# Performance work log

Measured on AMD Instinct MI355X. Metric: run time of the kernel, lower is better.

The kernel has to match this reference:

```python
import jax, jax.numpy as jnp
import numpy as np

B, T, D, H, F, E, K = 4, 1024, 1024, 16, 2048, 8, 2
LN_EPS = 1e-6  # flax LayerNorm default


def setup_inputs() -> dict:
    key = jax.random.key(0)
    ks = jax.random.split(key, 8)
    s = 0.02
    return {
        "x": jax.random.normal(ks[0], (B, T, D), jnp.float32),
        "ln1_scale": jnp.ones((D,), jnp.float32),
        "ln1_bias": jnp.zeros((D,), jnp.float32),
        "qkv_w": jax.random.normal(ks[1], (D, 3 * D), jnp.float32) * s,
        "qkv_b": jnp.zeros((3 * D,), jnp.float32),
        "out_w": jax.random.normal(ks[2], (D, D), jnp.float32) * s,
        "out_b": jnp.zeros((D,), jnp.float32),
        "ln2_scale": jnp.ones((D,), jnp.float32),
        "ln2_bias": jnp.zeros((D,), jnp.float32),
        "router_w": jax.random.normal(ks[3], (D, E), jnp.float32) * s,
        "w1": jax.random.normal(ks[4], (E, D, F), jnp.float32) * s,
        "b1": jnp.zeros((E, F), jnp.float32),
        "w2": jax.random.normal(ks[5], (E, F, D), jnp.float32) * s,
        "b2": jnp.zeros((E, D), jnp.float32),
    }


def _layernorm(x, scale, bias):
    mu = jnp.mean(x, axis=-1, keepdims=True)
    var = jnp.mean(jnp.square(x - mu), axis=-1, keepdims=True)
    return (x - mu) * jax.lax.rsqrt(var + LN_EPS) * scale + bias


def _attention(x, qkv_w, qkv_b, out_w, out_b):
    b, t, d = x.shape
    hd = d // H
    qkv = x @ qkv_w + qkv_b
    q, k, v = jnp.split(qkv, 3, axis=-1)
    q = q.reshape(b, t, H, hd).transpose(0, 2, 1, 3)  # (B,H,T,hd)
    k = k.reshape(b, t, H, hd).transpose(0, 2, 1, 3)
    v = v.reshape(b, t, H, hd).transpose(0, 2, 1, 3)
    scale = jnp.sqrt(jnp.float32(hd))
    scores = jnp.einsum("bhqd,bhkd->bhqk", q, k) / scale
    causal = jnp.triu(jnp.ones((t, t), jnp.bool_), k=1)
    scores = jnp.where(causal[None, None], -1e9, scores)
    attn = jax.nn.softmax(scores, axis=-1)
    out = jnp.einsum("bhqk,bhkd->bhqd", attn, v)
    out = out.transpose(0, 2, 1, 3).reshape(b, t, d)
    return out @ out_w + out_b


def _moe(x, router_w, w1, b1, w2, b2):
    b, t, d = x.shape
    logits = x @ router_w  # (B,T,E)
    probs = jax.nn.softmax(logits, axis=-1)
    topk_vals, topk_idx = jax.lax.top_k(logits, K)  # (B,T,K)
    gates = jax.nn.softmax(topk_vals, axis=-1)
    # aux load-balancing loss from top-1 dispatch
    dispatch = jax.nn.one_hot(topk_idx[..., 0], E, dtype=x.dtype)
    f = jnp.mean(dispatch, axis=(0, 1))
    P = jnp.mean(probs, axis=(0, 1))
    aux_loss = E * jnp.sum(f * P)
    # dense all-expert compute (faithful to original)
    h = jax.nn.gelu(jnp.einsum("btd,edf->ebtf", x, w1) + b1[:, None, None, :])
    eo = jnp.einsum("ebtf,efd->ebtd", h, w2) + b2[:, None, None, :]  # (E,B,T,D)
    bi = jnp.arange(b)[:, None, None]
    ti = jnp.arange(t)[None, :, None]
    selected = eo[topk_idx, bi, ti, :]  # (B,T,K,D)
    out = jnp.sum(gates[..., None] * selected, axis=2)
    return out, aux_loss


def reference(x, ln1_scale, ln1_bias, qkv_w, qkv_b, out_w, out_b,
              ln2_scale, ln2_bias, router_w, w1, b1, w2, b2):
    res = x
    h = _layernorm(x, ln1_scale, ln1_bias)
    h = _attention(h, qkv_w, qkv_b, out_w, out_b)
    x = h + res
    res = x
    hn = _layernorm(x, ln2_scale, ln2_bias)
    moe_out, aux_loss = _moe(hn, router_w, w1, b1, w2, b2)
    return moe_out + res, aux_loss
```

## Files before the change

### kernel.cpp

```cpp
#include <hip/hip_runtime.h>
#include <hip/hip_bf16.h>

using bf16 = __hip_bfloat16;
typedef __attribute__((ext_vector_type(8))) short short8;
typedef __attribute__((ext_vector_type(4))) float f32x4;

__device__ __forceinline__ unsigned short f2bu(float x) {
  union { bf16 b; unsigned short u; } cv; cv.b = __float2bfloat16(x); return cv.u;
}

__device__ __forceinline__ void gload_lds16(const bf16* g, bf16* l) {
  __builtin_amdgcn_global_load_lds(
      (const __attribute__((address_space(1))) void*)g,
      (__attribute__((address_space(3))) void*)l, 16, 0, 0);
}

__global__ __launch_bounds__(256) void transpose_to_bf16(
    const float* __restrict__ in, bf16* __restrict__ out, int R, int C) {
  __shared__ float tile[64][65];
  size_t bo = (size_t)blockIdx.z * R * C;
  in += bo; out += bo;
  int c0 = blockIdx.x * 64, r0 = blockIdx.y * 64;
  int tx = threadIdx.x & 15, ty = threadIdx.x >> 4;
#pragma unroll
  for (int i = 0; i < 4; ++i) {
    float4 v = *(const float4*)&in[(size_t)(r0 + ty + i * 16) * C + c0 + tx * 4];
    tile[ty + i * 16][tx * 4 + 0] = v.x;
    tile[ty + i * 16][tx * 4 + 1] = v.y;
    tile[ty + i * 16][tx * 4 + 2] = v.z;
    tile[ty + i * 16][tx * 4 + 3] = v.w;
  }
  __syncthreads();
  int c = threadIdx.x >> 2;
  int rg = (threadIdx.x & 3) * 16;
#pragma unroll
  for (int j = 0; j < 4; ++j) {
    ushort4 o;
    o.x = f2bu(tile[rg + j * 4 + 0][c]);
    o.y = f2bu(tile[rg + j * 4 + 1][c]);
    o.z = f2bu(tile[rg + j * 4 + 2][c]);
    o.w = f2bu(tile[rg + j * 4 + 3][c]);
    *(ushort4*)&out[(size_t)(c0 + c) * R + r0 + rg + j * 4] = o;
  }
}

__global__ __launch_bounds__(256) void ln_kernel(
    const float* __restrict__ in, const float* __restrict__ sc,
    const float* __restrict__ bi, bf16* __restrict__ out) {
  int row = blockIdx.x, tid = threadIdx.x;
  const float4* xr = (const float4*)(in + (size_t)row * 1024);
  float4 v = xr[tid];
  float s = v.x + v.y + v.z + v.w;
  float sq = v.x * v.x + v.y * v.y + v.z * v.z + v.w * v.w;
#pragma unroll
  for (int m = 1; m < 64; m <<= 1) { s += __shfl_xor(s, m); sq += __shfl_xor(sq, m); }
  __shared__ float red[8];
  int wid = tid >> 6, lane = tid & 63;
  if (lane == 0) { red[wid] = s; red[4 + wid] = sq; }
  __syncthreads();
  s = red[0] + red[1] + red[2] + red[3];
  sq = red[4] + red[5] + red[6] + red[7];
  float mu = s * (1.f / 1024.f);
  float rstd = rsqrtf(sq * (1.f / 1024.f) - mu * mu + 1e-6f);
  float4 scv = ((const float4*)sc)[tid];
  float4 biv = ((const float4*)bi)[tid];
  ushort4 ov;
  ov.x = f2bu((v.x - mu) * rstd * scv.x + biv.x);
  ov.y = f2bu((v.y - mu) * rstd * scv.y + biv.y);
  ov.z = f2bu((v.z - mu) * rstd * scv.z + biv.z);
  ov.w = f2bu((v.w - mu) * rstd * scv.w + biv.w);
  ((ushort4*)(out + (size_t)row * 1024))[tid] = ov;
}

template <int BM, int BN, int EPI, bool GATHER, bool GROUPED>
__global__ __launch_bounds__(256) void gemm_bt(
    const bf16* __restrict__ A, const bf16* __restrict__ B,
    const float* __restrict__ bias, const float* __restrict__ resid,
    void* __restrict__ C, bf16* __restrict__ VT, const int* __restrict__ gidx,
    const int* __restrict__ counts, const int* __restrict__ offsets,
    int M, int N, int K) {
  constexpr int FM = BM / 32;
  constexpr int FN = BN / 32;
  constexpr int AL = BM / 32;
  constexpr int BL = BN / 32;
  int e = blockIdx.z;
  int Mcnt = M, base = 0;
  if (GROUPED) { Mcnt = counts[e]; base = offsets[e]; }
  int m0 = blockIdx.y * BM, n0 = blockIdx.x * BN;
  if (m0 >= Mcnt) return;
  const bf16* Bp = B + (size_t)e * N * K;
  const float* biasp = bias + (size_t)e * N;
  __shared__ __align__(16) bf16 As[BM * 64];
  __shared__ __align__(16) bf16 Bs[BN * 64];
  int tid = threadIdx.x, lane = tid & 63, wid = tid >> 6;
  int lr = lane & 15, lg = lane >> 4;
  int wr = (wid >> 1) * (BM / 2), wc = (wid & 1) * (BN / 2);
  const bf16* aptr[AL];
  const bf16* bptr[BL];
  int adst[AL], bdst[BL];
#pragma unroll
  for (int i = 0; i < AL; ++i) {
    int idx = i * 256 + tid;
    int r = idx >> 3, cb = idx & 7;
    int cbs = cb ^ (r & 7);
    int gr = m0 + r;
    int cl = gr < Mcnt ? gr : (Mcnt - 1);
    size_t arow = GATHER ? (size_t)gidx[base + cl] : (size_t)(base + cl);
    aptr[i] = A + arow * K + cbs * 8;
    adst[i] = idx * 8;
  }
#pragma unroll
  for (int i = 0; i < BL; ++i) {
    int idx = i * 256 + tid;
    int r = idx >> 3, cb = idx & 7;
    int cbs = cb ^ (r & 7);
    bptr[i] = Bp + (size_t)(n0 + r) * K + cbs * 8;
    bdst[i] = idx * 8;
  }
  int xa = lr & 7;
  int colk[2];
  colk[0] = (lg ^ xa) * 8;
  colk[1] = ((lg + 4) ^ xa) * 8;
  int arow_lds[FM], brow_lds[FN];
#pragma unroll
  for (int m_ = 0; m_ < FM; ++m_) arow_lds[m_] = (wr + m_ * 16 + lr) * 64;
#pragma unroll
  for (int n_ = 0; n_ < FN; ++n_) brow_lds[n_] = (wc + n_ * 16 + lr) * 64;

  f32x4 acc[FM][FN] = {};
  int nt = K >> 6;
  for (int t = 0; t < nt; ++t) {
    __syncthreads();
    int k0 = t << 6;
#pragma unroll
    for (int i = 0; i < AL; ++i) gload_lds16(aptr[i] + k0, &As[adst[i]]);
#pragma unroll
    for (int i = 0; i < BL; ++i) gload_lds16(bptr[i] + k0, &Bs[bdst[i]]);
    __syncthreads();
#pragma unroll
    for (int h = 0; h < 2; ++h) {
      short8 af[FM], bfg[FN];
#pragma unroll
      for (int m_ = 0; m_ < FM; ++m_)
        af[m_] = *(const short8*)&As[arow_lds[m_] + colk[h]];
#pragma unroll
      for (int n_ = 0; n_ < FN; ++n_)
        bfg[n_] = *(const short8*)&Bs[brow_lds[n_] + colk[h]];
#pragma unroll
      for (int m_ = 0; m_ < FM; ++m_)
#pragma unroll
        for (int n_ = 0; n_ < FN; ++n_)
          acc[m_][n_] = __builtin_amdgcn_mfma_f32_16x16x32_bf16(af[m_], bfg[n_], acc[m_][n_], 0, 0, 0);
    }
  }
#pragma unroll
  for (int n_ = 0; n_ < FN; ++n_) {
    int acol = n0 + wc + n_ * 16 + lr;
    float bv = biasp[acol];
#pragma unroll
    for (int m_ = 0; m_ < FM; ++m_) {
      int rbase = m0 + wr + m_ * 16 + lg * 4;
#pragma unroll
      for (int q = 0; q < 4; ++q) {
        int gr = rbase + q;
        if (gr >= Mcnt) continue;
        size_t crow = (size_t)(base + gr);
        float v = acc[m_][n_][q] + bv;
        if (EPI == 1) {
          float z = 0.7978845608028654f * (v + 0.044715f * v * v * v);
          float t2 = __expf(2.f * z);
          v = v * (t2 / (t2 + 1.f));
          ((bf16*)C)[crow * N + acol] = __float2bfloat16(v);
        } else if (EPI == 2) {
          ((float*)C)[crow * N + acol] = v + resid[crow * N + acol];
        } else if (EPI == 3) {
          if (acol < 2048) {
            ((bf16*)C)[crow * N + acol] = __float2bfloat16(v);
          } else {
            int dg = acol - 2048;
            int hh = dg >> 6, dd = dg & 63;
            int bb = (int)(crow >> 10), tt = (int)(crow & 1023);
            VT[(((size_t)bb * 16 + hh) * 64 + dd) * 1024 + tt] = __float2bfloat16(v);
          }
        } else {
          ((bf16*)C)[crow * N + acol] = __float2bfloat16(v);
        }
      }
    }
  }
}

__global__ __launch_bounds__(256) void attn_kernel(const bf16* __restrict__ qkv,
                                                   const bf16* __restrict__ vt,
                                                   bf16* __restrict__ out) {
  constexpr int T = 1024, QS = 3072;
  int bh = blockIdx.y;
  int b = bh >> 4, h = bh & 15;
  __shared__ __align__(16) bf16 Ks[64][72];
  __shared__ __align__(16) bf16 Vs[64][72];
  __shared__ __align__(16) bf16 Pl[4][16][72];
  int tid = threadIdx.x, lane = tid & 63, wid = tid >> 6;
  int lr = lane & 15, lg = lane >> 4;
  const size_t rowb = (size_t)b * T;
  const float SC = 0.18033688011112042f;
  int sr[2], scb[2];
  const bf16* kbase[2];
  const bf16* vbase[2];
#pragma unroll
  for (int i = 0; i < 2; ++i) {
    int idx = tid + i * 256;
    sr[i] = idx >> 3; scb[i] = idx & 7;
    kbase[i] = qkv + (rowb + sr[i]) * QS + 1024 + h * 64 + scb[i] * 8;
    vbase[i] = vt + ((size_t)bh * 64 + sr[i]) * T + scb[i] * 8;
  }
  for (int half = 0; half < 2; ++half) {
    int qt = (half == 0) ? blockIdx.x : (15 - blockIdx.x);
    int qrow0 = qt * 64 + wid * 16 + lg * 4;
    const bf16* qp = qkv + (rowb + qt * 64 + wid * 16 + lr) * QS + h * 64;
    short8 qf0 = *(const short8*)(qp + lg * 8);
    short8 qf1 = *(const short8*)(qp + 32 + lg * 8);
    f32x4 o[4] = {};
    float mrow[4] = {-3e38f, -3e38f, -3e38f, -3e38f};
    float lrow[4] = {0.f, 0.f, 0.f, 0.f};
    short8 kreg[2], vreg[2];
#pragma unroll
    for (int i = 0; i < 2; ++i) {
      kreg[i] = *(const short8*)kbase[i];
      vreg[i] = *(const short8*)vbase[i];
    }
    for (int kv = 0; kv <= qt; ++kv) {
      __syncthreads();
#pragma unroll
      for (int i = 0; i < 2; ++i) {
        *(short8*)&Ks[sr[i]][scb[i] * 8] = kreg[i];
        *(short8*)&Vs[sr[i]][scb[i] * 8] = vreg[i];
      }
      __syncthreads();
      if (kv < qt) {
#pragma unroll
        for (int i = 0; i < 2; ++i) {
          kreg[i] = *(const short8*)(kbase[i] + (size_t)(kv + 1) * 64 * QS);
          vreg[i] = *(const short8*)(vbase[i] + (kv + 1) * 64);
        }
      }
      f32x4 s[4];
#pragma unroll
      for (int nf = 0; nf < 4; ++nf) {
        f32x4 z = {0.f, 0.f, 0.f, 0.f};
        short8 k0 = *(const short8*)&Ks[nf * 16 + lr][lg * 8];
        short8 k1 = *(const short8*)&Ks[nf * 16 + lr][32 + lg * 8];
        z = __builtin_amdgcn_mfma_f32_16x16x32_bf16(qf0, k0, z, 0, 0, 0);
        z = __builtin_amdgcn_mfma_f32_16x16x32_bf16(qf1, k1, z, 0, 0, 0);
        s[nf] = z;
      }
      bool diag = (kv == qt);
#pragma unroll
      for (int nf = 0; nf < 4; ++nf)
#pragma unroll
        for (int q = 0; q < 4; ++q) {
          float v = s[nf][q] * SC;
          if (diag) { int key = kv * 64 + nf * 16 + lr; if (key > qrow0 + q) v = -1e9f; }
          s[nf][q] = v;
        }
      float rs[4], resc[4];
#pragma unroll
      for (int q = 0; q < 4; ++q) {
        float v = fmaxf(fmaxf(s[0][q], s[1][q]), fmaxf(s[2][q], s[3][q]));
        v = fmaxf(v, __shfl_xor(v, 1));
        v = fmaxf(v, __shfl_xor(v, 2));
        v = fmaxf(v, __shfl_xor(v, 4));
        v = fmaxf(v, __shfl_xor(v, 8));
        float mn = fmaxf(mrow[q], v);
        resc[q] = __builtin_amdgcn_exp2f(mrow[q] - mn);
        mrow[q] = mn;
        rs[q] = 0.f;
      }
#pragma unroll
      for (int nf = 0; nf < 4; ++nf)
#pragma unroll
        for (int q = 0; q < 4; ++q) {
          float p = __builtin_amdgcn_exp2f(s[nf][q] - mrow[q]);
          rs[q] += p;
          Pl[wid][lg * 4 + q][nf * 16 + lr] = __float2bfloat16(p);
        }
#pragma unroll
      for (int q = 0; q < 4; ++q) {
        float v = rs[q];
        v += __shfl_xor(v, 1); v += __shfl_xor(v, 2);
        v += __shfl_xor(v, 4); v += __shfl_xor(v, 8);
        lrow[q] = lrow[q] * resc[q] + v;
        o[0][q] *= resc[q]; o[1][q] *= resc[q]; o[2][q] *= resc[q]; o[3][q] *= resc[q];
      }
      short8 pa0 = *(const short8*)&Pl[wid][lr][lg * 8];
      short8 pa1 = *(const short8*)&Pl[wid][lr][32 + lg * 8];
#pragma unroll
      for (int nf = 0; nf < 4; ++nf) {
        short8 v0 = *(const short8*)&Vs[nf * 16 + lr][lg * 8];
        short8 v1 = *(const short8*)&Vs[nf * 16 + lr][32 + lg * 8];
        o[nf] = __builtin_amdgcn_mfma_f32_16x16x32_bf16(pa0, v0, o[nf], 0, 0, 0);
        o[nf] = __builtin_amdgcn_mfma_f32_16x16x32_bf16(pa1, v1, o[nf], 0, 0, 0);
      }
    }
#pragma unroll
    for (int q = 0; q < 4; ++q) {
      float inv = 1.0f / lrow[q];
      size_t row = rowb + qrow0 + q;
#pragma unroll
      for (int nf = 0; nf < 4; ++nf)
        out[row * 1024 + h * 64 + nf * 16 + lr] = __float2bfloat16(o[nf][q] * inv);
    }
  }
}

__global__ __launch_bounds__(64) void router_kernel(
    const float* __restrict__ x2, const float* __restrict__ sc,
    const float* __restrict__ bi, const float* __restrict__ rw,
    bf16* __restrict__ ln2h, float* __restrict__ probs,
    int* __restrict__ topk, float* __restrict__ gates) {
  int t = blockIdx.x, lane = threadIdx.x;
  const float* xr = x2 + (size_t)t * 1024;
  float xv[16];
  float s = 0.f, sq = 0.f;
#pragma unroll
  for (int i = 0; i < 4; ++i) {
    float4 v = ((const float4*)xr)[lane * 4 + i];
    xv[i * 4 + 0] = v.x; xv[i * 4 + 1] = v.y; xv[i * 4 + 2] = v.z; xv[i * 4 + 3] = v.w;
    s += v.x + v.y + v.z + v.w;
    sq += v.x * v.x + v.y * v.y + v.z * v.z + v.w * v.w;
  }
#pragma unroll
  for (int m = 1; m < 64; m <<= 1) { s += __shfl_xor(s, m); sq += __shfl_xor(sq, m); }
  float mu = s * (1.f / 1024.f);
  float rstd = rsqrtf(sq * (1.f / 1024.f) - mu * mu + 1e-6f);
  float a8[8] = {};
  short8 o0, o1;
#pragma unroll
  for (int i = 0; i < 16; ++i) {
    int d = lane * 16 + i;
    float y = (xv[i] - mu) * rstd * sc[d] + bi[d];
    if (i < 8) o0[i] = (short)f2bu(y); else o1[i - 8] = (short)f2bu(y);
    const float4* rr = (const float4*)(rw + (size_t)d * 8);
    float4 r0 = rr[0], r1 = rr[1];
    a8[0] += y * r0.x; a8[1] += y * r0.y; a8[2] += y * r0.z; a8[3] += y * r0.w;
    a8[4] += y * r1.x; a8[5] += y * r1.y; a8[6] += y * r1.z; a8[7] += y * r1.w;
  }
  *(short8*)&ln2h[(size_t)t * 1024 + lane * 16] = o0;
  *(short8*)&ln2h[(size_t)t * 1024 + lane * 16 + 8] = o1;
#pragma unroll
  for (int m = 1; m < 64; m <<= 1)
#pragma unroll
    for (int e = 0; e < 8; ++e) a8[e] += __shfl_xor(a8[e], m);
  if (lane == 0) {
    float mx = a8[0];
#pragma unroll
    for (int e = 1; e < 8; ++e) mx = fmaxf(mx, a8[e]);
    float ps = 0.f, pe[8];
#pragma unroll
    for (int e = 0; e < 8; ++e) { pe[e] = expf(a8[e] - mx); ps += pe[e]; }
    float inv = 1.f / ps;
#pragma unroll
    for (int e = 0; e < 8; ++e) probs[t * 8 + e] = pe[e] * inv;
    int i0 = 0; float v0 = a8[0];
#pragma unroll
    for (int e = 1; e < 8; ++e) if (a8[e] > v0) { v0 = a8[e]; i0 = e; }
    int i1 = -1; float v1 = -3e38f;
#pragma unroll
    for (int e = 0; e < 8; ++e) if (e != i0 && a8[e] > v1) { v1 = a8[e]; i1 = e; }
    float g1 = 1.f / (1.f + expf(v0 - v1));
    topk[t * 2] = i0; topk[t * 2 + 1] = i1;
    gates[t * 2] = 1.f - g1; gates[t * 2 + 1] = g1;
  }
}

__global__ void count_kernel(const int* __restrict__ topk, int* __restrict__ counts,
                             int* __restrict__ offsets) {
  __shared__ int c[8];
  int tid = threadIdx.x;
  if (tid < 8) c[tid] = 0;
  __syncthreads();
  for (int p = tid; p < 8192; p += 256) atomicAdd(&c[topk[p]], 1);
  __syncthreads();
  if (tid == 0) {
    int off = 0;
    for (int e = 0; e < 8; ++e) { counts[e] = c[e]; offsets[e] = off; off += c[e]; }
  }
}

__global__ __launch_bounds__(256) void assign_kernel(
    const int* __restrict__ topk, const int* __restrict__ offsets,
    int* __restrict__ rows_tok, int* __restrict__ pair_pos) {
  int e = blockIdx.x;
  int tid = threadIdx.x, lane = tid & 63, wid = tid >> 6;
  int base = offsets[e];
  __shared__ int wsum[4];
  int run = 0;
  for (int start = 0; start < 8192; start += 256) {
    int p = start + tid;
    int f = (topk[p] == e) ? 1 : 0;
    int v = f;
#pragma unroll
    for (int o_ = 1; o_ < 64; o_ <<= 1) { int u = __shfl_up(v, o_); if (lane >= o_) v += u; }
    if (lane == 63) wsum[wid] = v;
    __syncthreads();
    int wbase = 0;
#pragma unroll
    for (int w = 0; w < 4; ++w) if (w < wid) wbase += wsum[w];
    int tot = wsum[0] + wsum[1] + wsum[2] + wsum[3];
    if (f) {
      int pos = base + run + wbase + v - 1;
      rows_tok[pos] = p >> 1;
      pair_pos[p] = pos;
    }
    run += tot;
    __syncthreads();
  }
}

__global__ __launch_bounds__(256) void combine_kernel(
    const float* __restrict__ x2, const bf16* __restrict__ eo,
    const float* __restrict__ gates, const int* __restrict__ pair_pos,
    float* __restrict__ out) {
  int t = blockIdx.x, tid = threadIdx.x;
  float g0 = gates[t * 2], g1 = gates[t * 2 + 1];
  size_t p0 = (size_t)pair_pos[t * 2] * 1024, p1 = (size_t)pair_pos[t * 2 + 1] * 1024;
  size_t rb = (size_t)t * 1024;
#pragma unroll
  for (int i = 0; i < 4; ++i) {
    int d = tid + i * 256;
    out[rb + d] = x2[rb + d] + g0 * __bfloat162float(eo[p0 + d]) + g1 * __bfloat162float(eo[p1 + d]);
  }
}

__global__ __launch_bounds__(256) void aux_kernel(const float* __restrict__ probs,
                                                  const int* __restrict__ topk,
                                                  float* __restrict__ out) {
  int tid = threadIdx.x, lane = tid & 63, wid = tid >> 6;
  float P[8] = {}, Fc[8] = {};
  for (int t = tid; t < 4096; t += 256) {
#pragma unroll
    for (int e = 0; e < 8; ++e) P[e] += probs[t * 8 + e];
    Fc[topk[t * 2]] += 1.f;
  }
#pragma unroll
  for (int m = 1; m < 64; m <<= 1)
#pragma unroll
    for (int e = 0; e < 8; ++e) { P[e] += __shfl_xor(P[e], m); Fc[e] += __shfl_xor(Fc[e], m); }
  __shared__ float sP[4][8], sF[4][8];
  if (lane == 0)
#pragma unroll
    for (int e = 0; e < 8; ++e) { sP[wid][e] = P[e]; sF[wid][e] = Fc[e]; }
  __syncthreads();
  if (tid == 0) {
    float aux = 0.f;
    for (int e = 0; e < 8; ++e) {
      float p = (sP[0][e] + sP[1][e] + sP[2][e] + sP[3][e]) * (1.f / 4096.f);
      float f = (sF[0][e] + sF[1][e] + sF[2][e] + sF[3][e]) * (1.f / 4096.f);
      aux += f * p;
    }
    out[0] = 8.f * aux;
  }
}

extern "C" void kernel_launch(void* const* d_in, const int* in_sizes, int n_in,
                              void* d_out, int out_size, void* d_ws, size_t ws_size,
                              hipStream_t stream) {
  (void)in_sizes; (void)n_in; (void)out_size; (void)ws_size;
  const float* x    = (const float*)d_in[0];
  const float* ln1s = (const float*)d_in[1];
  const float* ln1b = (const float*)d_in[2];
  const float* qkvw = (const float*)d_in[3];
  const float* qkvb = (const float*)d_in[4];
  const float* outw = (const float*)d_in[5];
  const float* outb = (const float*)d_in[6];
  const float* ln2s = (const float*)d_in[7];
  const float* ln2b = (const float*)d_in[8];
  const float* rw   = (const float*)d_in[9];
  const float* w1   = (const float*)d_in[10];
  const float* b1   = (const float*)d_in[11];
  const float* w2   = (const float*)d_in[12];
  const float* b2   = (const float*)d_in[13];

  char* ws = (char*)d_ws;
  size_t off = 0;
  auto alloc = [&](size_t bytes) -> char* {
    char* p = ws + off; off += (bytes + 255) & ~(size_t)255; return p;
  };
  bf16* qkvw_t  = (bf16*)alloc(3072ull * 1024 * 2);
  bf16* outw_t  = (bf16*)alloc(1024ull * 1024 * 2);
  bf16* w1_t    = (bf16*)alloc(8ull * 2048 * 1024 * 2);
  bf16* w2_t    = (bf16*)alloc(8ull * 1024 * 2048 * 2);
  bf16* h1      = (bf16*)alloc(4096ull * 1024 * 2);
  bf16* qkv     = (bf16*)alloc(4096ull * 3072 * 2);
  bf16* vtb     = (bf16*)alloc(64ull * 64 * 1024 * 2);
  bf16* attn_o  = (bf16*)alloc(4096ull * 1024 * 2);
  float* x2     = (float*)alloc(4096ull * 1024 * 4);
  bf16* ln2h    = (bf16*)alloc(4096ull * 1024 * 2);
  float* probs  = (float*)alloc(4096ull * 8 * 4);
  float* gates  = (float*)alloc(4096ull * 2 * 4);
  int* topk     = (int*)alloc(8192 * 4);
  int* counts   = (int*)alloc(64 * 4);
  int* offsets  = (int*)alloc(64 * 4);
  int* rows_tok = (int*)alloc(8192 * 4);
  int* pair_pos = (int*)alloc(8192 * 4);
  bf16* h_buf   = (bf16*)alloc(8192ull * 2048 * 2);
  bf16* eo      = (bf16*)alloc(8192ull * 1024 * 2);

  transpose_to_bf16<<<dim3(3072 / 64, 1024 / 64, 1), 256, 0, stream>>>(qkvw, qkvw_t, 1024, 3072);
  transpose_to_bf16<<<dim3(1024 / 64, 1024 / 64, 1), 256, 0, stream>>>(outw, outw_t, 1024, 1024);
  transpose_to_bf16<<<dim3(2048 / 64, 1024 / 64, 8), 256, 0, stream>>>(w1, w1_t, 1024, 2048);
  transpose_to_bf16<<<dim3(1024 / 64, 2048 / 64, 8), 256, 0, stream>>>(w2, w2_t, 2048, 1024);

  ln_kernel<<<4096, 256, 0, stream>>>(x, ln1s, ln1b, h1);

  gemm_bt<64, 128, 3, false, false><<<dim3(3072 / 128, 4096 / 64, 1), 256, 0, stream>>>(
      h1, qkvw_t, qkvb, nullptr, qkv, vtb, nullptr, nullptr, nullptr, 4096, 3072, 1024);

  attn_kernel<<<dim3(8, 64), 256, 0, stream>>>(qkv, vtb, attn_o);

  gemm_bt<64, 128, 2, false, false><<<dim3(1024 / 128, 4096 / 64, 1), 256, 0, stream>>>(
      attn_o, outw_t, outb, x, x2, nullptr, nullptr, nullptr, nullptr, 4096, 1024, 1024);

  router_kernel<<<4096, 64, 0, stream>>>(x2, ln2s, ln2b, rw, ln2h, probs, topk, gates);

  count_kernel<<<1, 256, 0, stream>>>(topk, counts, offsets);
  assign_kernel<<<8, 256, 0, stream>>>(topk, offsets, rows_tok, pair_pos);

  gemm_bt<64, 128, 1, true, true><<<dim3(2048 / 128, 8192 / 64, 8), 256, 0, stream>>>(
      ln2h, w1_t, b1, nullptr, h_buf, nullptr, rows_tok, counts, offsets, 8192, 2048, 1024);

  gemm_bt<64, 128, 0, false, true><<<dim3(1024 / 128, 8192 / 64, 8), 256, 0, stream>>>(
      h_buf, w2_t, b2, nullptr, eo, nullptr, nullptr, counts, offsets, 8192, 1024, 2048);

  combine_kernel<<<4096, 256, 0, stream>>>(x2, eo, gates, pair_pos, (float*)d_out);
  aux_kernel<<<1, 256, 0, stream>>>(probs, topk, (float*)d_out + 4194304);
}
```

Baseline: 365.5 us.

## Unpair attention query tiles and fuse small MoE bookkeeping kernels

The attention kernel no longer pairs query tiles qt and 15-qt in one block for load balance. It now launches one block per query tile (16x64 grid), which doubles the block count but makes the per-block work uneven under causal masking. The count kernel is folded into the assign kernel, with every block recomputing the expert histogram redundantly. The aux-loss kernel is folded into the combine kernel as an extra block. Together this removes two kernel launches at the cost of some duplicated histogram work.

```diff
diff --git a/kernel.cpp b/kernel.cpp
--- a/kernel.cpp
+++ b/kernel.cpp
@@ -213,102 +213,100 @@
     kbase[i] = qkv + (rowb + sr[i]) * QS + 1024 + h * 64 + scb[i] * 8;
     vbase[i] = vt + ((size_t)bh * 64 + sr[i]) * T + scb[i] * 8;
   }
-  for (int half = 0; half < 2; ++half) {
-    int qt = (half == 0) ? blockIdx.x : (15 - blockIdx.x);
-    int qrow0 = qt * 64 + wid * 16 + lg * 4;
-    const bf16* qp = qkv + (rowb + qt * 64 + wid * 16 + lr) * QS + h * 64;
-    short8 qf0 = *(const short8*)(qp + lg * 8);
-    short8 qf1 = *(const short8*)(qp + 32 + lg * 8);
-    f32x4 o[4] = {};
-    float mrow[4] = {-3e38f, -3e38f, -3e38f, -3e38f};
-    float lrow[4] = {0.f, 0.f, 0.f, 0.f};
-    short8 kreg[2], vreg[2];
+  int qt = blockIdx.x;
+  int qrow0 = qt * 64 + wid * 16 + lg * 4;
+  const bf16* qp = qkv + (rowb + qt * 64 + wid * 16 + lr) * QS + h * 64;
+  short8 qf0 = *(const short8*)(qp + lg * 8);
+  short8 qf1 = *(const short8*)(qp + 32 + lg * 8);
+  f32x4 o[4] = {};
+  float mrow[4] = {-3e38f, -3e38f, -3e38f, -3e38f};
+  float lrow[4] = {0.f, 0.f, 0.f, 0.f};
+  short8 kreg[2], vreg[2];
+#pragma unroll
+  for (int i = 0; i < 2; ++i) {
+    kreg[i] = *(const short8*)kbase[i];
+    vreg[i] = *(const short8*)vbase[i];
+  }
+  for (int kv = 0; kv <= qt; ++kv) {
+    __syncthreads();
 #pragma unroll
     for (int i = 0; i < 2; ++i) {
-      kreg[i] = *(const short8*)kbase[i];
-      vreg[i] = *(const short8*)vbase[i];
-    }
-    for (int kv = 0; kv <= qt; ++kv) {
-      __syncthreads();
+      *(short8*)&Ks[sr[i]][scb[i] * 8] = kreg[i];
+      *(short8*)&Vs[sr[i]][scb[i] * 8] = vreg[i];
+    }
+    __syncthreads();
+    if (kv < qt) {
 #pragma unroll
       for (int i = 0; i < 2; ++i) {
-        *(short8*)&Ks[sr[i]][scb[i] * 8] = kreg[i];
-        *(short8*)&Vs[sr[i]][scb[i] * 8] = vreg[i];
+        kreg[i] = *(const short8*)(kbase[i] + (size_t)(kv + 1) * 64 * QS);
+        vreg[i] = *(const short8*)(vbase[i] + (kv + 1) * 64);
       }
-      __syncthreads();
-      if (kv < qt) {
-#pragma unroll
-        for (int i = 0; i < 2; ++i) {
-          kreg[i] = *(const short8*)(kbase[i] + (size_t)(kv + 1) * 64 * QS);
-          vreg[i] = *(const short8*)(vbase[i] + (kv + 1) * 64);
-        }
+    }
+    f32x4 s[4];
+#pragma unroll
+    for (int nf = 0; nf < 4; ++nf) {
+      f32x4 z = {0.f, 0.f, 0.f, 0.f};
+      short8 k0 = *(const short8*)&Ks[nf * 16 + lr][lg * 8];
+      short8 k1 = *(const short8*)&Ks[nf * 16 + lr][32 + lg * 8];
+      z = __builtin_amdgcn_mfma_f32_16x16x32_bf16(qf0, k0, z, 0, 0, 0);
+      z = __builtin_amdgcn_mfma_f32_16x16x32_bf16(qf1, k1, z, 0, 0, 0);
+      s[nf] = z;
+    }
+    bool diag = (kv == qt);
+#pragma unroll
+    for (int nf = 0; nf < 4; ++nf)
+#pragma unroll
+      for (int q = 0; q < 4; ++q) {
+        float v = s[nf][q] * SC;
+        if (diag) { int key = kv * 64 + nf * 16 + lr; if (key > qrow0 + q) v = -1e9f; }
+        s[nf][q] = v;
       }
-      f32x4 s[4];
-#pragma unroll
-      for (int nf = 0; nf < 4; ++nf) {
-        f32x4 z = {0.f, 0.f, 0.f, 0.f};
-        short8 k0 = *(const short8*)&Ks[nf * 16 + lr][lg * 8];
-        short8 k1 = *(const short8*)&Ks[nf * 16 + lr][32 + lg * 8];
-        z = __builtin_amdgcn_mfma_f32_16x16x32_bf16(qf0, k0, z, 0, 0, 0);
-        z = __builtin_amdgcn_mfma_f32_16x16x32_bf16(qf1, k1, z, 0, 0, 0);
-        s[nf] = z;
+    float rs[4], resc[4];
+#pragma unroll
+    for (int q = 0; q < 4; ++q) {
+      float v = fmaxf(fmaxf(s[0][q], s[1][q]), fmaxf(s[2][q], s[3][q]));
+      v = fmaxf(v, __shfl_xor(v, 1));
+      v = fmaxf(v, __shfl_xor(v, 2));
+      v = fmaxf(v, __shfl_xor(v, 4));
+      v = fmaxf(v, __shfl_xor(v, 8));
+      float mn = fmaxf(mrow[q], v);
+      resc[q] = __builtin_amdgcn_exp2f(mrow[q] - mn);
+      mrow[q] = mn;
+      rs[q] = 0.f;
+    }
+#pragma unroll
+    for (int nf = 0; nf < 4; ++nf)
+#pragma unroll
+      for (int q = 0; q < 4; ++q) {
+        float p = __builtin_amdgcn_exp2f(s[nf][q] - mrow[q]);
+        rs[q] += p;
+        Pl[wid][lg * 4 + q][nf * 16 + lr] = __float2bfloat16(p);
       }
-      bool diag = (kv == qt);
-#pragma unroll
-      for (int nf = 0; nf < 4; ++nf)
-#pragma unroll
-        for (int q = 0; q < 4; ++q) {
-          float v = s[nf][q] * SC;
-          if (diag) { int key = kv * 64 + nf * 16 + lr; if (key > qrow0 + q) v = -1e9f; }
-          s[nf][q] = v;
-        }
-      float rs[4], resc[4];
-#pragma unroll
-      for (int q = 0; q < 4; ++q) {
-        float v = fmaxf(fmaxf(s[0][q], s[1][q]), fmaxf(s[2][q], s[3][q]));
-        v = fmaxf(v, __shfl_xor(v, 1));
-        v = fmaxf(v, __shfl_xor(v, 2));
-        v = fmaxf(v, __shfl_xor(v, 4));
-        v = fmaxf(v, __shfl_xor(v, 8));
-        float mn = fmaxf(mrow[q], v);
-        resc[q] = __builtin_amdgcn_exp2f(mrow[q] - mn);
-        mrow[q] = mn;
-        rs[q] = 0.f;
-      }
-#pragma unroll
-      for (int nf = 0; nf < 4; ++nf)
-#pragma unroll
-        for (int q = 0; q < 4; ++q) {
-          float p = __builtin_amdgcn_exp2f(s[nf][q] - mrow[q]);
-          rs[q] += p;
-          Pl[wid][lg * 4 + q][nf * 16 + lr] = __float2bfloat16(p);
-        }
-#pragma unroll
-      for (int q = 0; q < 4; ++q) {
-        float v = rs[q];
-        v += __shfl_xor(v, 1); v += __shfl_xor(v, 2);
-        v += __shfl_xor(v, 4); v += __shfl_xor(v, 8);
-        lrow[q] = lrow[q] * resc[q] + v;
-        o[0][q] *= resc[q]; o[1][q] *= resc[q]; o[2][q] *= resc[q]; o[3][q] *= resc[q];
-      }
-      short8 pa0 = *(const short8*)&Pl[wid][lr][lg * 8];
-      short8 pa1 = *(const short8*)&Pl[wid][lr][32 + lg * 8];
-#pragma unroll
-      for (int nf = 0; nf < 4; ++nf) {
-        short8 v0 = *(const short8*)&Vs[nf * 16 + lr][lg * 8];
-        short8 v1 = *(const short8*)&Vs[nf * 16 + lr][32 + lg * 8];
-        o[nf] = __builtin_amdgcn_mfma_f32_16x16x32_bf16(pa0, v0, o[nf], 0, 0, 0);
-        o[nf] = __builtin_amdgcn_mfma_f32_16x16x32_bf16(pa1, v1, o[nf], 0, 0, 0);
-      }
-    }
 #pragma unroll
     for (int q = 0; q < 4; ++q) {
-      float inv = 1.0f / lrow[q];
-      size_t row = rowb + qrow0 + q;
-#pragma unroll
-      for (int nf = 0; nf < 4; ++nf)
-        out[row * 1024 + h * 64 + nf * 16 + lr] = __float2bfloat16(o[nf][q] * inv);
-    }
+      float v = rs[q];
+      v += __shfl_xor(v, 1); v += __shfl_xor(v, 2);
+      v += __shfl_xor(v, 4); v += __shfl_xor(v, 8);
+      lrow[q] = lrow[q] * resc[q] + v;
+      o[0][q] *= resc[q]; o[1][q] *= resc[q]; o[2][q] *= resc[q]; o[3][q] *= resc[q];
+    }
+    short8 pa0 = *(const short8*)&Pl[wid][lr][lg * 8];
+    short8 pa1 = *(const short8*)&Pl[wid][lr][32 + lg * 8];
+#pragma unroll
+    for (int nf = 0; nf < 4; ++nf) {
+      short8 v0 = *(const short8*)&Vs[nf * 16 + lr][lg * 8];
+      short8 v1 = *(const short8*)&Vs[nf * 16 + lr][32 + lg * 8];
+      o[nf] = __builtin_amdgcn_mfma_f32_16x16x32_bf16(pa0, v0, o[nf], 0, 0, 0);
+      o[nf] = __builtin_amdgcn_mfma_f32_16x16x32_bf16(pa1, v1, o[nf], 0, 0, 0);
+    }
+  }
+#pragma unroll
+  for (int q = 0; q < 4; ++q) {
+    float inv = 1.0f / lrow[q];
+    size_t row = rowb + qrow0 + q;
+#pragma unroll
+    for (int nf = 0; nf < 4; ++nf)
+      out[row * 1024 + h * 64 + nf * 16 + lr] = __float2bfloat16(o[nf][q] * inv);
   }
 }
 
@@ -372,26 +370,20 @@
   }
 }
 
-__global__ void count_kernel(const int* __restrict__ topk, int* __restrict__ counts,
-                             int* __restrict__ offsets) {
+__global__ __launch_bounds__(256) void assign_kernel(
+    const int* __restrict__ topk, int* __restrict__ counts,
+    int* __restrict__ offsets, int* __restrict__ rows_tok,
+    int* __restrict__ pair_pos) {
+  int e = blockIdx.x;
+  int tid = threadIdx.x, lane = tid & 63, wid = tid >> 6;
   __shared__ int c[8];
-  int tid = threadIdx.x;
   if (tid < 8) c[tid] = 0;
   __syncthreads();
   for (int p = tid; p < 8192; p += 256) atomicAdd(&c[topk[p]], 1);
   __syncthreads();
-  if (tid == 0) {
-    int off = 0;
-    for (int e = 0; e < 8; ++e) { counts[e] = c[e]; offsets[e] = off; off += c[e]; }
-  }
-}
-
-__global__ __launch_bounds__(256) void assign_kernel(
-    const int* __restrict__ topk, const int* __restrict__ offsets,
-    int* __restrict__ rows_tok, int* __restrict__ pair_pos) {
-  int e = blockIdx.x;
-  int tid = threadIdx.x, lane = tid & 63, wid = tid >> 6;
-  int base = offsets[e];
+  int base = 0;
+  for (int k = 0; k < 8; ++k) if (k < e) base += c[k];
+  if (tid == 0) { counts[e] = c[e]; offsets[e] = base; }
   __shared__ int wsum[4];
   int run = 0;
   for (int start = 0; start < 8192; start += 256) {
@@ -419,8 +411,37 @@
 __global__ __launch_bounds__(256) void combine_kernel(
     const float* __restrict__ x2, const bf16* __restrict__ eo,
     const float* __restrict__ gates, const int* __restrict__ pair_pos,
-    float* __restrict__ out) {
+    const float* __restrict__ probs, const int* __restrict__ topk,
+    float* __restrict__ out, float* __restrict__ aux_out) {
   int t = blockIdx.x, tid = threadIdx.x;
+  if (t == 4096) {
+    int lane = tid & 63, wid = tid >> 6;
+    float P[8] = {}, Fc[8] = {};
+    for (int tt = tid; tt < 4096; tt += 256) {
+#pragma unroll
+      for (int e = 0; e < 8; ++e) P[e] += probs[tt * 8 + e];
+      Fc[topk[tt * 2]] += 1.f;
+    }
+#pragma unroll
+    for (int m = 1; m < 64; m <<= 1)
+#pragma unroll
+      for (int e = 0; e < 8; ++e) { P[e] += __shfl_xor(P[e], m); Fc[e] += __shfl_xor(Fc[e], m); }
+    __shared__ float sP[4][8], sF[4][8];
+    if (lane == 0)
+#pragma unroll
+      for (int e = 0; e < 8; ++e) { sP[wid][e] = P[e]; sF[wid][e] = Fc[e]; }
+    __syncthreads();
+    if (tid == 0) {
+      float aux = 0.f;
+      for (int e = 0; e < 8; ++e) {
+        float p = (sP[0][e] + sP[1][e] + sP[2][e] + sP[3][e]) * (1.f / 4096.f);
+        float f = (sF[0][e] + sF[1][e] + sF[2][e] + sF[3][e]) * (1.f / 4096.f);
+        aux += f * p;
+      }
+      aux_out[0] = 8.f * aux;
+    }
+    return;
+  }
   float g0 = gates[t * 2], g1 = gates[t * 2 + 1];
   size_t p0 = (size_t)pair_pos[t * 2] * 1024, p1 = (size_t)pair_pos[t * 2 + 1] * 1024;
   size_t rb = (size_t)t * 1024;
@@ -428,36 +449,6 @@
   for (int i = 0; i < 4; ++i) {
     int d = tid + i * 256;
     out[rb + d] = x2[rb + d] + g0 * __bfloat162float(eo[p0 + d]) + g1 * __bfloat162float(eo[p1 + d]);
-  }
-}
-
-__global__ __launch_bounds__(256) void aux_kernel(const float* __restrict__ probs,
-                                                  const int* __restrict__ topk,
-                                                  float* __restrict__ out) {
-  int tid = threadIdx.x, lane = tid & 63, wid = tid >> 6;
-  float P[8] = {}, Fc[8] = {};
-  for (int t = tid; t < 4096; t += 256) {
-#pragma unroll
-    for (int e = 0; e < 8; ++e) P[e] += probs[t * 8 + e];
-    Fc[topk[t * 2]] += 1.f;
-  }
-#pragma unroll
-  for (int m = 1; m < 64; m <<= 1)
-#pragma unroll
-    for (int e = 0; e < 8; ++e) { P[e] += __shfl_xor(P[e], m); Fc[e] += __shfl_xor(Fc[e], m); }
-  __shared__ float sP[4][8], sF[4][8];
-  if (lane == 0)
-#pragma unroll
-    for (int e = 0; e < 8; ++e) { sP[wid][e] = P[e]; sF[wid][e] = Fc[e]; }
-  __syncthreads();
-  if (tid == 0) {
-    float aux = 0.f;
-    for (int e = 0; e < 8; ++e) {
-      float p = (sP[0][e] + sP[1][e] + sP[2][e] + sP[3][e]) * (1.f / 4096.f);
-      float f = (sF[0][e] + sF[1][e] + sF[2][e] + sF[3][e]) * (1.f / 4096.f);
-      aux += f * p;
-    }
-    out[0] = 8.f * aux;
   }
 }
 
@@ -515,15 +506,14 @@
   gemm_bt<64, 128, 3, false, false><<<dim3(3072 / 128, 4096 / 64, 1), 256, 0, stream>>>(
       h1, qkvw_t, qkvb, nullptr, qkv, vtb, nullptr, nullptr, nullptr, 4096, 3072, 1024);
 
-  attn_kernel<<<dim3(8, 64), 256, 0, stream>>>(qkv, vtb, attn_o);
+  attn_kernel<<<dim3(16, 64), 256, 0, stream>>>(qkv, vtb, attn_o);
 
   gemm_bt<64, 128, 2, false, false><<<dim3(1024 / 128, 4096 / 64, 1), 256, 0, stream>>>(
       attn_o, outw_t, outb, x, x2, nullptr, nullptr, nullptr, nullptr, 4096, 1024, 1024);
 
   router_kernel<<<4096, 64, 0, stream>>>(x2, ln2s, ln2b, rw, ln2h, probs, topk, gates);
 
-  count_kernel<<<1, 256, 0, stream>>>(topk, counts, offsets);
-  assign_kernel<<<8, 256, 0, stream>>>(topk, offsets, rows_tok, pair_pos);
+  assign_kernel<<<8, 256, 0, stream>>>(topk, counts, offsets, rows_tok, pair_pos);
 
   gemm_bt<64, 128, 1, true, true><<<dim3(2048 / 128, 8192 / 64, 8), 256, 0, stream>>>(
       ln2h, w1_t, b1, nullptr, h_buf, nullptr, rows_tok, counts, offsets, 8192, 2048, 1024);
@@ -531,6 +521,6 @@
   gemm_bt<64, 128, 0, false, true><<<dim3(1024 / 128, 8192 / 64, 8), 256, 0, stream>>>(
       h_buf, w2_t, b2, nullptr, eo, nullptr, nullptr, counts, offsets, 8192, 1024, 2048);
 
-  combine_kernel<<<4096, 256, 0, stream>>>(x2, eo, gates, pair_pos, (float*)d_out);
-  aux_kernel<<<1, 256, 0, stream>>>(probs, topk, (float*)d_out + 4194304);
-}
+  combine_kernel<<<4097, 256, 0, stream>>>(x2, eo, gates, pair_pos, probs, topk,
+                                           (float*)d_out, (float*)d_out + 4194304);
+}
```

Result: slower. 377.4 us (+3.2%).
